# Kernel tuning notes

Measured on AMD Instinct MI355X. Metric: run time of the kernel, lower is better.

## Reference

```python
import jax, jax.numpy as jnp
import numpy as np

P = 1024   # total patches = B * n_patches
B = 32
NPATCH = 32
D = 64
EPS = 1e-6


def _mlp2(x, W1, b1, W2, b2):
    # Linear -> ReLU -> (Dropout p=0) -> Linear
    return jax.nn.relu(x @ W1 + b1) @ W2 + b2


def setup_inputs() -> dict:
    key = jax.random.key(0)
    ks = jax.random.split(key, 32)
    d = D
    inp = {}
    inp['x'] = jax.random.normal(ks[0], (65536, d), dtype=jnp.float32)
    inp['subgraphs_nodes_mapper'] = jax.random.randint(ks[1], (65536,), 0, 65536)
    inp['subgraphs_batch'] = jnp.sort(jax.random.randint(ks[2], (65536,), 0, P))
    inp['subgraphs_batch_row'] = jax.random.randint(ks[3], (16384,), 0, P)
    inp['subgraphs_batch_col'] = jax.random.randint(ks[4], (16384,), 0, P)
    inp['coarsen_edge_attr'] = jax.random.uniform(ks[5], (16384,), dtype=jnp.float32)
    s = 1.0 / np.sqrt(d)
    def W(k, shape):
        return jax.random.normal(k, shape, dtype=jnp.float32) * s
    # input_transform (Linear,ReLU,Linear,ReLU)
    inp['Wt1'] = W(ks[6], (d, d)); inp['bt1'] = jnp.zeros((d,), jnp.float32)
    inp['Wt2'] = W(ks[7], (d, d)); inp['bt2'] = jnp.zeros((d,), jnp.float32)
    # pre / post deepset (2 layers each)
    inp['Wpre1'] = W(ks[8], (d, d)); inp['bpre1'] = jnp.zeros((d,), jnp.float32)
    inp['Wpre2'] = W(ks[9], (d, d)); inp['bpre2'] = jnp.zeros((d,), jnp.float32)
    inp['Wpost1'] = W(ks[10], (d, d)); inp['bpost1'] = jnp.zeros((d,), jnp.float32)
    inp['Wpost2'] = W(ks[11], (d, d)); inp['bpost2'] = jnp.zeros((d,), jnp.float32)
    # linK / linV
    inp['Wk'] = W(ks[12], (d, d)); inp['bk'] = jnp.zeros((d,), jnp.float32)
    inp['Wv'] = W(ks[13], (d, d)); inp['bv'] = jnp.zeros((d,), jnp.float32)
    # attention-based readout seed
    inp['seed'] = jax.random.normal(ks[14], (d,), dtype=jnp.float32)
    # classifier: Linear(d, d//2), ReLU, Linear(d//2, num_classes)
    inp['Wc1'] = W(ks[15], (d, d // 2)); inp['bc1'] = jnp.zeros((d // 2,), jnp.float32)
    inp['Wc2'] = W(ks[16], (d // 2, 10)); inp['bc2'] = jnp.zeros((10,), jnp.float32)
    return inp


def reference(x, subgraphs_nodes_mapper, subgraphs_batch, subgraphs_batch_row,
              subgraphs_batch_col, coarsen_edge_attr,
              Wt1, bt1, Wt2, bt2,
              Wpre1, bpre1, Wpre2, bpre2,
              Wpost1, bpost1, Wpost2, bpost2,
              Wk, bk, Wv, bv, seed,
              Wc1, bc1, Wc2, bc2):
    seg = jax.ops.segment_sum
    row, col, batch = subgraphs_batch_row, subgraphs_batch_col, subgraphs_batch

    # input_transform then gather onto subgraph-combined node set
    h = jax.nn.relu(jax.nn.relu(x @ Wt1 + bt1) @ Wt2 + bt2)
    hs = h[subgraphs_nodes_mapper]                        # [N, d]

    # symmetric random-walk normalization of coarsened edge weights
    deg = seg(coarsen_edge_attr, row, num_segments=P)
    dinv = jnp.where(deg > 0, jax.lax.rsqrt(jnp.maximum(deg, EPS)), 0.0)
    attr = dinv[row] * coarsen_edge_attr * dinv[col]      # [E]

    # Q: pre-deepset -> scatter-sum per patch -> post-deepset
    Q = _mlp2(hs, Wpre1, bpre1, Wpre2, bpre2)
    Qs = seg(Q, batch, num_segments=P)                    # [P, d]
    Qs = _mlp2(Qs, Wpost1, bpost1, Wpost2, bpost2)

    # K: linear proj, scatter-mean per patch; V: linear proj (node level)
    K = hs @ Wk + bk
    cnt = seg(jnp.ones_like(K[:, 0]), batch, num_segments=P)
    Ks = seg(K, batch, num_segments=P) / jnp.maximum(cnt, 1.0)[:, None]
    V = hs @ Wv + bv

    # relu kernel feature maps
    Qk = jax.nn.relu(Qs)                                  # [P, d]
    Kk = jax.nn.relu(K)                                   # [N, d]
    Ksk = jax.nn.relu(Ks)                                 # [P, d]

    # linear attention state per patch: M_p = sum_{i in p} k_i v_i^T
    M = seg(Kk[:, :, None] * V[:, None, :], batch, num_segments=P)  # [P, d, d]
    # random-walk message / key propagation on coarsened patch graph
    M = M + seg(attr[:, None, None] * M[col], row, num_segments=P)
    Kagg = Ksk + seg(attr[:, None] * Ksk[col], row, num_segments=P)

    # kernelized attention readout per patch
    num = jnp.einsum('pd,pde->pe', Qk, M)
    den = jnp.sum(Qk * Kagg, axis=-1)
    out = num / (den[:, None] + EPS)                      # [P, d]

    # (B p) d -> B p d, attention-based set readout with learned seed
    out = out.reshape(B, NPATCH, D)
    scores = jax.nn.softmax((out @ seed) / jnp.sqrt(jnp.float32(D)), axis=1)
    pooled = jnp.einsum('bp,bpd->bd', scores, out)        # [B, d]

    # classifier
    logits = jax.nn.relu(pooled @ Wc1 + bc1) @ Wc2 + bc2  # [B, num_classes]
    return logits
```

## Files before the change

kernel.cpp:

```cpp
#include <hip/hip_runtime.h>
#include <cstddef>

#define NND  65536
#define PP   1024
#define EE   16384
#define CAP  88
#define TJ2  32
#define EPSF 1e-6f

typedef unsigned int   u32;
typedef unsigned short u16;
typedef __attribute__((ext_vector_type(8))) short bf16x8;
typedef __attribute__((ext_vector_type(4))) float f32x4;

__device__ __forceinline__ u16 f2bf(float f) {
    u32 u = __float_as_uint(f);
    u += 0x7fffu + ((u >> 16) & 1u);
    return (u16)(u >> 16);
}
__device__ __forceinline__ float bflo(u32 u) { return __uint_as_float(u << 16); }
__device__ __forceinline__ float bfhi(u32 u) { return __uint_as_float(u & 0xffff0000u); }
__device__ __forceinline__ float bf1(u16 v)  { return __uint_as_float(((u32)v) << 16); }
__device__ __forceinline__ u32 relu2(u32 v) {
    u32 mask = ((v & 0x80008000u) >> 15) * 0xFFFFu;
    return v & ~mask;
}


__global__ void patch_bounds_kernel(const int* __restrict__ batch, int* __restrict__ start) {
    int i = blockIdx.x * blockDim.x + threadIdx.x;
    if (i >= NND) return;
    int b  = batch[i];
    int bp = (i == 0) ? -1 : batch[i - 1];
    for (int p = bp + 1; p <= b; ++p) start[p] = i;
    if (i == NND - 1) {
        for (int p = b + 1; p <= PP; ++p) start[p] = NND;
    }
}

__global__ void edge_hist_kernel(const int* __restrict__ row, const int* __restrict__ col,
                                 const float* __restrict__ attr,
                                 float* __restrict__ deg, int* __restrict__ colcnt) {
    int e = blockIdx.x * blockDim.x + threadIdx.x;
    if (e >= EE) return;
    atomicAdd(&deg[row[e]], attr[e]);
    atomicAdd(&colcnt[col[e]], 1);
}

__global__ void scan_dinv_kernel(const int* __restrict__ colcnt, int* __restrict__ col_start,
                                 const float* __restrict__ deg, float* __restrict__ dinv) {
    __shared__ int s[PP];
    int t = threadIdx.x;
    s[t] = colcnt[t];
    float dg = deg[t];
    dinv[t] = (dg > 0.f) ? rsqrtf(fmaxf(dg, EPSF)) : 0.f;
    __syncthreads();
    for (int off = 1; off < PP; off <<= 1) {
        int v = (t >= off) ? s[t - off] : 0;
        __syncthreads();
        s[t] += v;
        __syncthreads();
    }
    col_start[t + 1] = s[t];
    if (t == 0) col_start[0] = 0;
}

__global__ void edge_scatter_kernel(const int* __restrict__ col, const int* __restrict__ col_start,
                                    int* __restrict__ colfill, int* __restrict__ edge_perm) {
    int e = blockIdx.x * blockDim.x + threadIdx.x;
    if (e >= EE) return;
    int c = col[e];
    int pos = col_start[c] + atomicAdd(&colfill[c], 1);
    edge_perm[pos] = e;
}

__global__ __launch_bounds__(256)
void pack_w_kernel(const float* W0, const float* W1, const float* W2, const float* W3,
                   const float* W4, const float* W5, const float* W6, const float* W7,
                   u16* __restrict__ out) {
    const float* Ws[8] = {W0, W1, W2, W3, W4, W5, W6, W7};
    const float* W = Ws[blockIdx.x];
    u16* dst = out + (size_t)blockIdx.x * 4096;
    int t = threadIdx.x;
    for (int idx = t; idx < 512; idx += 256) {
        int f = idx >> 6, l = idx & 63;
        int kk = f >> 2, nt = f & 3;
        int g = l >> 4, m = l & 15;
#pragma unroll
        for (int j = 0; j < 8; ++j) {
            int k = kk * 32 + g * 8 + j;
            int n = nt * 16 + m;
            dst[idx * 8 + j] = f2bf(W[k * 64 + n]);
        }
    }
}


__device__ __forceinline__ void stage_f32(const float* __restrict__ in, u16* s, int row0, int t) {
    int r = t >> 2, c = t & 3;
    const float4* src = (const float4*)(in + (size_t)(row0 + r) * 64 + c * 16);
    char* sb = (char*)s + r * 128;
    int swz = (r & 7) << 4;
#pragma unroll
    for (int q4 = 0; q4 < 4; ++q4) {
        float4 v = src[q4];
        u32 p0 = (u32)f2bf(v.x) | ((u32)f2bf(v.y) << 16);
        u32 p1 = (u32)f2bf(v.z) | ((u32)f2bf(v.w) << 16);
        int pc = c * 8 + q4 * 2;
        *(u32*)(sb + ((pc * 4) ^ swz))       = p0;
        *(u32*)(sb + (((pc + 1) * 4) ^ swz)) = p1;
    }
}

__device__ __forceinline__ void stage_bf16_gather(const u16* __restrict__ h,
                                                  const int* __restrict__ gmap,
                                                  u16* s, int row0, int t) {
    int r = t >> 2, c = t & 3;
    int sr = gmap[row0 + r];
    const uint4* src = (const uint4*)(h + (size_t)sr * 64) + c * 2;
    uint4 a = src[0], b = src[1];
    char* sb = (char*)s + r * 128;
    int swz = (r & 7) << 4;
    *(uint4*)(sb + ((c * 32) ^ swz))      = a;
    *(uint4*)(sb + ((c * 32 + 16) ^ swz)) = b;
}

template <bool RELU>
__device__ __forceinline__ void gemm_layer(const u16* src, u16* dst,
                                           const u16* __restrict__ Wp,
                                           const float* __restrict__ bias,
                                           int wv, int lane) {
    int g = lane >> 4, m = lane & 15;
    int arow = wv * 16 + m;
    const char* sb = (const char*)src + arow * 128;
    int aswz = (arow & 7) << 4;
    bf16x8 a0 = *(const bf16x8*)(sb + ((g * 16) ^ aswz));
    bf16x8 a1 = *(const bf16x8*)(sb + ((64 + g * 16) ^ aswz));
    const bf16x8* wp = (const bf16x8*)Wp;
#pragma unroll
    for (int ntile = 0; ntile < 4; ++ntile) {
        float bv = bias[ntile * 16 + m];
        f32x4 acc = {bv, bv, bv, bv};
        acc = __builtin_amdgcn_mfma_f32_16x16x32_bf16(a0, wp[(0 * 4 + ntile) * 64 + lane], acc, 0, 0, 0);
        acc = __builtin_amdgcn_mfma_f32_16x16x32_bf16(a1, wp[(1 * 4 + ntile) * 64 + lane], acc, 0, 0, 0);
        int col = ntile * 16 + m;
#pragma unroll
        for (int rg = 0; rg < 4; ++rg) {
            float v = acc[rg];
            if (RELU) v = fmaxf(v, 0.f);
            int rr = wv * 16 + g * 4 + rg;
            *(u16*)((char*)dst + rr * 128 + ((2 * col) ^ ((rr & 7) << 4))) = f2bf(v);
        }
    }
}

__device__ __forceinline__ void copy_out_bf16(const u16* s, u16* __restrict__ g, int row0, int t) {
    int r = t >> 2, c = t & 3;
    const char* sb = (const char*)s + r * 128;
    int swz = (r & 7) << 4;
    uint4 a = *(const uint4*)(sb + ((c * 32) ^ swz));
    uint4 b = *(const uint4*)(sb + ((c * 32 + 16) ^ swz));
    uint4* dst = (uint4*)(g + (size_t)(row0 + r) * 64) + c * 2;
    dst[0] = a; dst[1] = b;
}

__global__ __launch_bounds__(256)
void mfma_mlp2_kernel(const float* __restrict__ in,
                      const u16* __restrict__ Wp1, const float* __restrict__ b1,
                      const u16* __restrict__ Wp2, const float* __restrict__ b2,
                      u16* __restrict__ out) {
    __shared__ __align__(16) u16 xs[4096];
    __shared__ __align__(16) u16 ys[4096];
    int t = threadIdx.x, lane = t & 63, wv = t >> 6;
    int row0 = blockIdx.x * 64;
    stage_f32(in, xs, row0, t);
    gemm_layer<true>(xs, ys, Wp1, b1, wv, lane);
    gemm_layer<true>(ys, xs, Wp2, b2, wv, lane);
    copy_out_bf16(xs, out, row0, t);
}

__global__ __launch_bounds__(256)
void qkv_mfma_kernel(const u16* __restrict__ h, const int* __restrict__ gmap,
                     const u16* __restrict__ Wpk, const float* __restrict__ bk,
                     const u16* __restrict__ Wpv, const float* __restrict__ bv,
                     const u16* __restrict__ Wp1, const float* __restrict__ bp1,
                     const u16* __restrict__ Wp2, const float* __restrict__ bp2,
                     u16* __restrict__ Kout, u16* __restrict__ Vout, u16* __restrict__ Qout) {
    __shared__ __align__(16) u16 xs[4096];
    __shared__ __align__(16) u16 ys[4096];
    int t = threadIdx.x, lane = t & 63, wv = t >> 6;
    int row0 = blockIdx.x * 64;
    stage_bf16_gather(h, gmap, xs, row0, t);
    gemm_layer<false>(xs, ys, Wpk, bk, wv, lane);
    copy_out_bf16(ys, Kout, row0, t);
    gemm_layer<false>(xs, ys, Wpv, bv, wv, lane);
    copy_out_bf16(ys, Vout, row0, t);
    gemm_layer<true>(xs, ys, Wp1, bp1, wv, lane);
    gemm_layer<false>(ys, xs, Wp2, bp2, wv, lane);
    copy_out_bf16(xs, Qout, row0, t);
}

__global__ __launch_bounds__(256)
void patch_reduce_kernel(const u16* __restrict__ Qn, const u16* __restrict__ K,
                         const int* __restrict__ start,
                         float* __restrict__ Qs_raw, float* __restrict__ Ksk) {
    __shared__ float qred[8][64], kred[8][64];
    int p = blockIdx.x, t = threadIdx.x;
    int w = t & 31, s = t >> 5;
    int i0 = start[p], i1 = start[p + 1];
    float qa0 = 0.f, qa1 = 0.f, ka0 = 0.f, ka1 = 0.f;
    for (int i = i0 + s; i < i1; i += 8) {
        u32 qv = ((const u32*)(Qn + (size_t)i * 64))[w];
        u32 kv = ((const u32*)(K  + (size_t)i * 64))[w];
        qa0 += bflo(qv); qa1 += bfhi(qv);
        ka0 += bflo(kv); ka1 += bfhi(kv);
    }
    qred[s][w * 2] = qa0; qred[s][w * 2 + 1] = qa1;
    kred[s][w * 2] = ka0; kred[s][w * 2 + 1] = ka1;
    __syncthreads();
    if (t < 64) {
        float q = 0.f, k = 0.f;
#pragma unroll
        for (int z = 0; z < 8; ++z) { q += qred[z][t]; k += kred[z][t]; }
        Qs_raw[(size_t)p * 64 + t] = q;
        int cnt = i1 - i0;
        Ksk[(size_t)p * 64 + t] = fmaxf(k / (float)max(cnt, 1), 0.f);
    }
}

__global__ __launch_bounds__(256)
void attn2_kernel(const u16* __restrict__ Qkb, const u16* __restrict__ Kb,
                  const u16* __restrict__ Vb, const float* __restrict__ Kskb,
                  const int* __restrict__ e_row, const float* __restrict__ e_attr,
                  const int* __restrict__ edge_perm, const int* __restrict__ col_start,
                  const int* __restrict__ patch_start, const float* __restrict__ dinv,
                  float* __restrict__ num, float* __restrict__ Kagg) {
    __shared__ u16   Ks[CAP * 66];
    __shared__ u16   Vs[CAP * 66];
    __shared__ u16   Qs[TJ2 * 66];
    __shared__ float accS[TJ2 * 64];
    __shared__ float dots[4][CAP];
    __shared__ float coef[TJ2];
    __shared__ int   trow[TJ2];
    __shared__ float Ksc[64];
    int c = blockIdx.x, t = threadIdx.x, wv = t >> 6, lane = t & 63;
    int e0 = col_start[c], e1 = col_start[c + 1];
    int ntgt = e1 - e0 + 1;
    int i0 = patch_start[c], i1 = patch_start[c + 1];
    float dc = dinv[c];
    if (t < 64) Ksc[t] = Kskb[(size_t)c * 64 + t];

    for (int tc = 0; tc < ntgt; tc += TJ2) {
        int mj = min(TJ2, ntgt - tc);
        __syncthreads();
        if (t < mj) {
            int j = tc + t; int p; float cf;
            if (j == 0) { p = c; cf = 1.f; }
            else { int e = edge_perm[e0 + j - 1]; p = e_row[e]; cf = dinv[p] * e_attr[e] * dc; }
            trow[t] = p; coef[t] = cf;
        }
        for (int idx = t; idx < mj * 64; idx += 256) accS[idx] = 0.f;
        __syncthreads();
        for (int idx = t; idx < mj * 32; idx += 256) {
            int j = idx >> 5, q = idx & 31;
            u32 v = ((const u32*)(Qkb + (size_t)trow[j] * 64))[q];
            *(u32*)&Qs[j * 66 + q * 2] = v;
        }
        for (int ic = i0; ic < i1; ic += CAP) {
            int nc = min(CAP, i1 - ic);
            __syncthreads();
            for (int idx = t; idx < nc * 8; idx += 256) {
                int i = idx >> 3, q = idx & 7;
                uint4 kv = *((const uint4*)(Kb + (size_t)(ic + i) * 64) + q);
                uint4 vv = *((const uint4*)(Vb + (size_t)(ic + i) * 64) + q);
                u32* kd = (u32*)&Ks[i * 66 + q * 8];
                kd[0] = relu2(kv.x); kd[1] = relu2(kv.y);
                kd[2] = relu2(kv.z); kd[3] = relu2(kv.w);
                u32* vd = (u32*)&Vs[i * 66 + q * 8];
                vd[0] = vv.x; vd[1] = vv.y; vd[2] = vv.z; vd[3] = vv.w;
            }
            __syncthreads();
            for (int j = wv; j < mj; j += 4) {
                for (int ib = 0; ib < nc; ib += 64) {
                    int i = ib + lane;
                    if (i < nc) {
                        float dot = 0.f;
                        const u32* kr = (const u32*)&Ks[i * 66];
                        const u32* qr = (const u32*)&Qs[j * 66];
#pragma unroll 8
                        for (int q = 0; q < 32; ++q) {
                            u32 kw = kr[q], qw = qr[q];
                            dot = fmaf(bflo(qw), bflo(kw), dot);
                            dot = fmaf(bfhi(qw), bfhi(kw), dot);
                        }
                        dots[wv][i] = dot;
                    }
                }
                float out = 0.f;
#pragma unroll 4
                for (int i = 0; i < nc; ++i)
                    out = fmaf(dots[wv][i], bf1(Vs[i * 66 + lane]), out);
                accS[j * 64 + lane] += out;
            }
        }
        __syncthreads();
        for (int idx = t; idx < mj * 64; idx += 256) {
            int j = idx >> 6, d = idx & 63;
            float cf = coef[j];
            atomicAdd(&num[(size_t)trow[j] * 64 + d],  cf * accS[j * 64 + d]);
            atomicAdd(&Kagg[(size_t)trow[j] * 64 + d], cf * Ksc[d]);
        }
    }
}

__global__ __launch_bounds__(64)
void final_kernel(const float* __restrict__ num, const u16* __restrict__ Qk,
                  const float* __restrict__ Kagg, const float* __restrict__ seed,
                  const float* __restrict__ Wc1, const float* __restrict__ bc1,
                  const float* __restrict__ Wc2, const float* __restrict__ bc2,
                  float* __restrict__ logits) {
    __shared__ float s_out[32][65];
    __shared__ float s_rd[32], s_sc[32], s_pool[64], s_c1[32], s_seed[64];
    int b = blockIdx.x, t = threadIdx.x;
    s_seed[t] = seed[t];
    if (t < 32) {
        int p = b * 32 + t;
        float den = 0.f;
        for (int d = 0; d < 64; ++d)
            den = fmaf(bf1(Qk[(size_t)p * 64 + d]), Kagg[(size_t)p * 64 + d], den);
        s_rd[t] = 1.f / (den + EPSF);
    }
    __syncthreads();
    for (int p = 0; p < 32; ++p)
        s_out[p][t] = num[(size_t)(b * 32 + p) * 64 + t] * s_rd[p];
    __syncthreads();
    if (t < 32) {
        float sc = 0.f;
        for (int d = 0; d < 64; ++d) sc = fmaf(s_out[t][d], s_seed[d], sc);
        s_sc[t] = sc * 0.125f;
    }
    __syncthreads();
    if (t == 0) {
        float mx = -1e30f;
        for (int p = 0; p < 32; ++p) mx = fmaxf(mx, s_sc[p]);
        float sm = 0.f;
        for (int p = 0; p < 32; ++p) { float e = expf(s_sc[p] - mx); s_sc[p] = e; sm += e; }
        float inv = 1.f / sm;
        for (int p = 0; p < 32; ++p) s_sc[p] *= inv;
    }
    __syncthreads();
    {
        float pa = 0.f;
        for (int p = 0; p < 32; ++p) pa = fmaf(s_sc[p], s_out[p][t], pa);
        s_pool[t] = pa;
    }
    __syncthreads();
    if (t < 32) {
        float a = bc1[t];
        for (int d = 0; d < 64; ++d) a = fmaf(s_pool[d], Wc1[d * 32 + t], a);
        s_c1[t] = fmaxf(a, 0.f);
    }
    __syncthreads();
    if (t < 10) {
        float a = bc2[t];
        for (int j = 0; j < 32; ++j) a = fmaf(s_c1[j], Wc2[j * 10 + t], a);
        logits[b * 10 + t] = a;
    }
}


extern "C" void kernel_launch(void* const* d_in, const int* in_sizes, int n_in,
                              void* d_out, int out_size, void* d_ws, size_t ws_size,
                              hipStream_t stream) {
    const float* x      = (const float*)d_in[0];
    const int*   mapper = (const int*)d_in[1];
    const int*   batch  = (const int*)d_in[2];
    const int*   e_row  = (const int*)d_in[3];
    const int*   e_col  = (const int*)d_in[4];
    const float* e_attr = (const float*)d_in[5];
    const float* Wt1 = (const float*)d_in[6],  *bt1 = (const float*)d_in[7];
    const float* Wt2 = (const float*)d_in[8],  *bt2 = (const float*)d_in[9];
    const float* Wpre1 = (const float*)d_in[10], *bpre1 = (const float*)d_in[11];
    const float* Wpre2 = (const float*)d_in[12], *bpre2 = (const float*)d_in[13];
    const float* Wpost1 = (const float*)d_in[14], *bpost1 = (const float*)d_in[15];
    const float* Wpost2 = (const float*)d_in[16], *bpost2 = (const float*)d_in[17];
    const float* Wk = (const float*)d_in[18], *bk = (const float*)d_in[19];
    const float* Wv = (const float*)d_in[20], *bv = (const float*)d_in[21];
    const float* seed = (const float*)d_in[22];
    const float* Wc1 = (const float*)d_in[23], *bc1 = (const float*)d_in[24];
    const float* Wc2 = (const float*)d_in[25], *bc2 = (const float*)d_in[26];
    float* logits = (float*)d_out;

    char* w = (char*)d_ws;
    const size_t NB2 = (size_t)NND * 64 * 2;
    u16* hb  = (u16*)w;             w += NB2;
    u16* Kb  = (u16*)w;             w += NB2;
    u16* Vb  = (u16*)w;             w += NB2;
    u16* Qnb = (u16*)w;             w += NB2;
    u16* Wp  = (u16*)w;             w += 8 * 4096 * 2;
    u16* Qkb = (u16*)w;             w += PP * 64 * 2;
    float* numb   = (float*)w;      w += PP * 64 * 4;
    float* Kagg   = (float*)w;      w += PP * 64 * 4;
    float* Qs_raw = (float*)w;      w += PP * 64 * 4;
    float* Kskb   = (float*)w;      w += PP * 64 * 4;
    float* deg    = (float*)w;      w += PP * 4;
    int*   colcnt = (int*)w;        w += PP * 4;
    int*   colfill= (int*)w;        w += PP * 4;
    float* dinv   = (float*)w;      w += PP * 4;
    int* patch_start = (int*)w;     w += (PP + 1) * 4;
    int* col_start   = (int*)w;     w += (PP + 1) * 4;
    int* edge_perm   = (int*)w;     w += EE * 4;

    hipMemsetAsync(numb, 0, 2 * PP * 64 * sizeof(float), stream);
    hipMemsetAsync(deg, 0, 3 * PP * sizeof(int), stream);

    patch_bounds_kernel<<<NND / 256, 256, 0, stream>>>(batch, patch_start);
    edge_hist_kernel<<<EE / 256, 256, 0, stream>>>(e_row, e_col, e_attr, deg, colcnt);
    scan_dinv_kernel<<<1, PP, 0, stream>>>(colcnt, col_start, deg, dinv);
    edge_scatter_kernel<<<EE / 256, 256, 0, stream>>>(e_col, col_start, colfill, edge_perm);

    pack_w_kernel<<<8, 256, 0, stream>>>(Wt1, Wt2, Wk, Wv, Wpre1, Wpre2, Wpost1, Wpost2, Wp);

    mfma_mlp2_kernel<<<NND / 64, 256, 0, stream>>>(
        x, Wp + 0 * 4096, bt1, Wp + 1 * 4096, bt2, hb);
    qkv_mfma_kernel<<<NND / 64, 256, 0, stream>>>(
        hb, mapper, Wp + 2 * 4096, bk, Wp + 3 * 4096, bv,
        Wp + 4 * 4096, bpre1, Wp + 5 * 4096, bpre2, Kb, Vb, Qnb);
    patch_reduce_kernel<<<PP, 256, 0, stream>>>(Qnb, Kb, patch_start, Qs_raw, Kskb);
    mfma_mlp2_kernel<<<PP / 64, 256, 0, stream>>>(
        Qs_raw, Wp + 6 * 4096, bpost1, Wp + 7 * 4096, bpost2, Qkb);
    attn2_kernel<<<PP, 256, 0, stream>>>(Qkb, Kb, Vb, Kskb, e_row, e_attr, edge_perm,
                                         col_start, patch_start, dinv, numb, Kagg);
    final_kernel<<<32, 64, 0, stream>>>(numb, Qkb, Kagg, seed, Wc1, bc1, Wc2, bc2, logits);
}
```

Before: 199.3 us.

## Fuse setup kernels and fold patch reductions into QKV GEMM epilogue

```diff
diff --git a/kernel.cpp b/kernel.cpp
--- a/kernel.cpp
+++ b/kernel.cpp
@@ -27,71 +27,73 @@
 }
 
 
-__global__ void patch_bounds_kernel(const int* __restrict__ batch, int* __restrict__ start) {
-    int i = blockIdx.x * blockDim.x + threadIdx.x;
-    if (i >= NND) return;
-    int b  = batch[i];
-    int bp = (i == 0) ? -1 : batch[i - 1];
-    for (int p = bp + 1; p <= b; ++p) start[p] = i;
-    if (i == NND - 1) {
-        for (int p = b + 1; p <= PP; ++p) start[p] = NND;
-    }
-}
-
-__global__ void edge_hist_kernel(const int* __restrict__ row, const int* __restrict__ col,
-                                 const float* __restrict__ attr,
-                                 float* __restrict__ deg, int* __restrict__ colcnt) {
-    int e = blockIdx.x * blockDim.x + threadIdx.x;
-    if (e >= EE) return;
-    atomicAdd(&deg[row[e]], attr[e]);
-    atomicAdd(&colcnt[col[e]], 1);
-}
-
-__global__ void scan_dinv_kernel(const int* __restrict__ colcnt, int* __restrict__ col_start,
-                                 const float* __restrict__ deg, float* __restrict__ dinv) {
-    __shared__ int s[PP];
+__global__ __launch_bounds__(256)
+void setup_a_kernel(const int* __restrict__ batch, int* __restrict__ start,
+                    const float* W0, const float* W1, const float* W2, const float* W3,
+                    const float* W4, const float* W5, const float* W6, const float* W7,
+                    u16* __restrict__ wout) {
+    int blk = blockIdx.x, t = threadIdx.x;
+    if (blk < 256) {
+        int i = blk * 256 + t;
+        int b  = batch[i];
+        int bp = (i == 0) ? -1 : batch[i - 1];
+        for (int p = bp + 1; p <= b; ++p) start[p] = i;
+        if (i == NND - 1) {
+            for (int p = b + 1; p <= PP; ++p) start[p] = NND;
+        }
+    } else {
+        const float* Ws[8] = {W0, W1, W2, W3, W4, W5, W6, W7};
+        const float* W = Ws[blk - 256];
+        u16* dst = wout + (size_t)(blk - 256) * 4096;
+        for (int idx = t; idx < 512; idx += 256) {
+            int f = idx >> 6, l = idx & 63;
+            int kk = f >> 2, nt = f & 3;
+            int g = l >> 4, m = l & 15;
+#pragma unroll
+            for (int j = 0; j < 8; ++j) {
+                int k = kk * 32 + g * 8 + j;
+                int n = nt * 16 + m;
+                dst[idx * 8 + j] = f2bf(W[k * 64 + n]);
+            }
+        }
+    }
+}
+
+
+__global__ __launch_bounds__(1024)
+void setup_edges_kernel(const int* __restrict__ e_row, const int* __restrict__ e_col,
+                        const float* __restrict__ e_attr,
+                        int* __restrict__ col_start, int* __restrict__ edge_perm,
+                        float* __restrict__ dinv_g) {
+    __shared__ float sdeg[PP];
+    __shared__ int scc[PP], sfc[PP], stmp[PP];
     int t = threadIdx.x;
-    s[t] = colcnt[t];
-    float dg = deg[t];
-    dinv[t] = (dg > 0.f) ? rsqrtf(fmaxf(dg, EPSF)) : 0.f;
+    sdeg[t] = 0.f; scc[t] = 0; sfc[t] = 0;
+    __syncthreads();
+    for (int e = t; e < EE; e += 1024) {
+        atomicAdd(&sdeg[e_row[e]], e_attr[e]);
+        atomicAdd(&scc[e_col[e]], 1);
+    }
+    __syncthreads();
+    float dg = sdeg[t];
+    dinv_g[t] = (dg > 0.f) ? rsqrtf(fmaxf(dg, EPSF)) : 0.f;
+    stmp[t] = scc[t];
     __syncthreads();
     for (int off = 1; off < PP; off <<= 1) {
-        int v = (t >= off) ? s[t - off] : 0;
+        int v = (t >= off) ? stmp[t - off] : 0;
         __syncthreads();
-        s[t] += v;
+        stmp[t] += v;
         __syncthreads();
     }
-    col_start[t + 1] = s[t];
+    col_start[t + 1] = stmp[t];
     if (t == 0) col_start[0] = 0;
-}
-
-__global__ void edge_scatter_kernel(const int* __restrict__ col, const int* __restrict__ col_start,
-                                    int* __restrict__ colfill, int* __restrict__ edge_perm) {
-    int e = blockIdx.x * blockDim.x + threadIdx.x;
-    if (e >= EE) return;
-    int c = col[e];
-    int pos = col_start[c] + atomicAdd(&colfill[c], 1);
-    edge_perm[pos] = e;
-}
-
-__global__ __launch_bounds__(256)
-void pack_w_kernel(const float* W0, const float* W1, const float* W2, const float* W3,
-                   const float* W4, const float* W5, const float* W6, const float* W7,
-                   u16* __restrict__ out) {
-    const float* Ws[8] = {W0, W1, W2, W3, W4, W5, W6, W7};
-    const float* W = Ws[blockIdx.x];
-    u16* dst = out + (size_t)blockIdx.x * 4096;
-    int t = threadIdx.x;
-    for (int idx = t; idx < 512; idx += 256) {
-        int f = idx >> 6, l = idx & 63;
-        int kk = f >> 2, nt = f & 3;
-        int g = l >> 4, m = l & 15;
-#pragma unroll
-        for (int j = 0; j < 8; ++j) {
-            int k = kk * 32 + g * 8 + j;
-            int n = nt * 16 + m;
-            dst[idx * 8 + j] = f2bf(W[k * 64 + n]);
-        }
+    int excl = stmp[t] - scc[t];
+    scc[t] = excl;
+    __syncthreads();
+    for (int e = t; e < EE; e += 1024) {
+        int c = e_col[e];
+        int pos = scc[c] + atomicAdd(&sfc[c], 1);
+        edge_perm[pos] = e;
     }
 }
 
@@ -164,11 +166,34 @@
     dst[0] = a; dst[1] = b;
 }
 
+__device__ __forceinline__ void seg_reduce_tile(const u16* tile, const int* __restrict__ batch,
+                                                int row0, int wv, int lane,
+                                                float* __restrict__ gout) {
+    float s = 0.f;
+    int cur = batch[row0 + wv * 16];
+#pragma unroll
+    for (int r = 0; r < 16; ++r) {
+        int row = wv * 16 + r;
+        const char* rb = (const char*)tile + row * 128;
+        float v = bf1(*(const u16*)(rb + ((2 * lane) ^ ((row & 7) << 4))));
+        int b = batch[row0 + row];
+        if (b != cur) {
+            atomicAdd(&gout[(size_t)cur * 64 + lane], s);
+            s = 0.f; cur = b;
+        }
+        s += v;
+    }
+    atomicAdd(&gout[(size_t)cur * 64 + lane], s);
+}
+
+template <bool KSK>
 __global__ __launch_bounds__(256)
 void mfma_mlp2_kernel(const float* __restrict__ in,
                       const u16* __restrict__ Wp1, const float* __restrict__ b1,
                       const u16* __restrict__ Wp2, const float* __restrict__ b2,
-                      u16* __restrict__ out) {
+                      u16* __restrict__ out,
+                      const int* __restrict__ pstart, const float* __restrict__ Ksum,
+                      u16* __restrict__ Kskb) {
     __shared__ __align__(16) u16 xs[4096];
     __shared__ __align__(16) u16 ys[4096];
     int t = threadIdx.x, lane = t & 63, wv = t >> 6;
@@ -177,15 +202,26 @@
     gemm_layer<true>(xs, ys, Wp1, b1, wv, lane);
     gemm_layer<true>(ys, xs, Wp2, b2, wv, lane);
     copy_out_bf16(xs, out, row0, t);
+    if (KSK) {
+        for (int idx = t; idx < 4096; idx += 256) {
+            int r = idx >> 6, d = idx & 63;
+            int p = row0 + r;
+            int cnt = pstart[p + 1] - pstart[p];
+            float kv = Ksum[(size_t)p * 64 + d] / (float)max(cnt, 1);
+            Kskb[(size_t)p * 64 + d] = f2bf(fmaxf(kv, 0.f));
+        }
+    }
 }
 
 __global__ __launch_bounds__(256)
 void qkv_mfma_kernel(const u16* __restrict__ h, const int* __restrict__ gmap,
+                     const int* __restrict__ batch,
                      const u16* __restrict__ Wpk, const float* __restrict__ bk,
                      const u16* __restrict__ Wpv, const float* __restrict__ bv,
                      const u16* __restrict__ Wp1, const float* __restrict__ bp1,
                      const u16* __restrict__ Wp2, const float* __restrict__ bp2,
-                     u16* __restrict__ Kout, u16* __restrict__ Vout, u16* __restrict__ Qout) {
+                     u16* __restrict__ Kout, u16* __restrict__ Vout,
+                     float* __restrict__ Qsum, float* __restrict__ Ksum) {
     __shared__ __align__(16) u16 xs[4096];
     __shared__ __align__(16) u16 ys[4096];
     int t = threadIdx.x, lane = t & 63, wv = t >> 6;
@@ -193,44 +229,17 @@
     stage_bf16_gather(h, gmap, xs, row0, t);
     gemm_layer<false>(xs, ys, Wpk, bk, wv, lane);
     copy_out_bf16(ys, Kout, row0, t);
+    seg_reduce_tile(ys, batch, row0, wv, lane, Ksum);
     gemm_layer<false>(xs, ys, Wpv, bv, wv, lane);
     copy_out_bf16(ys, Vout, row0, t);
     gemm_layer<true>(xs, ys, Wp1, bp1, wv, lane);
     gemm_layer<false>(ys, xs, Wp2, bp2, wv, lane);
-    copy_out_bf16(xs, Qout, row0, t);
-}
-
-__global__ __launch_bounds__(256)
-void patch_reduce_kernel(const u16* __restrict__ Qn, const u16* __restrict__ K,
-                         const int* __restrict__ start,
-                         float* __restrict__ Qs_raw, float* __restrict__ Ksk) {
-    __shared__ float qred[8][64], kred[8][64];
-    int p = blockIdx.x, t = threadIdx.x;
-    int w = t & 31, s = t >> 5;
-    int i0 = start[p], i1 = start[p + 1];
-    float qa0 = 0.f, qa1 = 0.f, ka0 = 0.f, ka1 = 0.f;
-    for (int i = i0 + s; i < i1; i += 8) {
-        u32 qv = ((const u32*)(Qn + (size_t)i * 64))[w];
-        u32 kv = ((const u32*)(K  + (size_t)i * 64))[w];
-        qa0 += bflo(qv); qa1 += bfhi(qv);
-        ka0 += bflo(kv); ka1 += bfhi(kv);
-    }
-    qred[s][w * 2] = qa0; qred[s][w * 2 + 1] = qa1;
-    kred[s][w * 2] = ka0; kred[s][w * 2 + 1] = ka1;
-    __syncthreads();
-    if (t < 64) {
-        float q = 0.f, k = 0.f;
-#pragma unroll
-        for (int z = 0; z < 8; ++z) { q += qred[z][t]; k += kred[z][t]; }
-        Qs_raw[(size_t)p * 64 + t] = q;
-        int cnt = i1 - i0;
-        Ksk[(size_t)p * 64 + t] = fmaxf(k / (float)max(cnt, 1), 0.f);
-    }
+    seg_reduce_tile(xs, batch, row0, wv, lane, Qsum);
 }
 
 __global__ __launch_bounds__(256)
 void attn2_kernel(const u16* __restrict__ Qkb, const u16* __restrict__ Kb,
-                  const u16* __restrict__ Vb, const float* __restrict__ Kskb,
+                  const u16* __restrict__ Vb, const u16* __restrict__ Kskb,
                   const int* __restrict__ e_row, const float* __restrict__ e_attr,
                   const int* __restrict__ edge_perm, const int* __restrict__ col_start,
                   const int* __restrict__ patch_start, const float* __restrict__ dinv,
@@ -248,7 +257,7 @@
     int ntgt = e1 - e0 + 1;
     int i0 = patch_start[c], i1 = patch_start[c + 1];
     float dc = dinv[c];
-    if (t < 64) Ksc[t] = Kskb[(size_t)c * 64 + t];
+    if (t < 64) Ksc[t] = bf1(Kskb[(size_t)c * 64 + t]);
 
     for (int tc = 0; tc < ntgt; tc += TJ2) {
         int mj = min(TJ2, ntgt - tc);
@@ -396,39 +405,33 @@
     u16* hb  = (u16*)w;             w += NB2;
     u16* Kb  = (u16*)w;             w += NB2;
     u16* Vb  = (u16*)w;             w += NB2;
-    u16* Qnb = (u16*)w;             w += NB2;
     u16* Wp  = (u16*)w;             w += 8 * 4096 * 2;
     u16* Qkb = (u16*)w;             w += PP * 64 * 2;
-    float* numb   = (float*)w;      w += PP * 64 * 4;
-    float* Kagg   = (float*)w;      w += PP * 64 * 4;
-    float* Qs_raw = (float*)w;      w += PP * 64 * 4;
-    float* Kskb   = (float*)w;      w += PP * 64 * 4;
-    float* deg    = (float*)w;      w += PP * 4;
-    int*   colcnt = (int*)w;        w += PP * 4;
-    int*   colfill= (int*)w;        w += PP * 4;
-    float* dinv   = (float*)w;      w += PP * 4;
+    u16* Kskb= (u16*)w;             w += PP * 64 * 2;
+    float* Qsum  = (float*)w;       w += PP * 64 * 4;
+    float* Ksum  = (float*)w;       w += PP * 64 * 4;
+    float* numb  = (float*)w;       w += PP * 64 * 4;
+    float* Kagg  = (float*)w;       w += PP * 64 * 4;
+    float* dinv  = (float*)w;       w += PP * 4;
     int* patch_start = (int*)w;     w += (PP + 1) * 4;
     int* col_start   = (int*)w;     w += (PP + 1) * 4;
     int* edge_perm   = (int*)w;     w += EE * 4;
 
-    hipMemsetAsync(numb, 0, 2 * PP * 64 * sizeof(float), stream);
-    hipMemsetAsync(deg, 0, 3 * PP * sizeof(int), stream);
-
-    patch_bounds_kernel<<<NND / 256, 256, 0, stream>>>(batch, patch_start);
-    edge_hist_kernel<<<EE / 256, 256, 0, stream>>>(e_row, e_col, e_attr, deg, colcnt);
-    scan_dinv_kernel<<<1, PP, 0, stream>>>(colcnt, col_start, deg, dinv);
-    edge_scatter_kernel<<<EE / 256, 256, 0, stream>>>(e_col, col_start, colfill, edge_perm);
-
-    pack_w_kernel<<<8, 256, 0, stream>>>(Wt1, Wt2, Wk, Wv, Wpre1, Wpre2, Wpost1, Wpost2, Wp);
-
-    mfma_mlp2_kernel<<<NND / 64, 256, 0, stream>>>(
-        x, Wp + 0 * 4096, bt1, Wp + 1 * 4096, bt2, hb);
+    hipMemsetAsync(Qsum, 0, 4 * PP * 64 * sizeof(float), stream);
+
+    setup_a_kernel<<<264, 256, 0, stream>>>(batch, patch_start,
+        Wt1, Wt2, Wk, Wv, Wpre1, Wpre2, Wpost1, Wpost2, Wp);
+    setup_edges_kernel<<<1, 1024, 0, stream>>>(e_row, e_col, e_attr,
+                                               col_start, edge_perm, dinv);
+
+    mfma_mlp2_kernel<false><<<NND / 64, 256, 0, stream>>>(
+        x, Wp + 0 * 4096, bt1, Wp + 1 * 4096, bt2, hb, nullptr, nullptr, nullptr);
     qkv_mfma_kernel<<<NND / 64, 256, 0, stream>>>(
-        hb, mapper, Wp + 2 * 4096, bk, Wp + 3 * 4096, bv,
-        Wp + 4 * 4096, bpre1, Wp + 5 * 4096, bpre2, Kb, Vb, Qnb);
-    patch_reduce_kernel<<<PP, 256, 0, stream>>>(Qnb, Kb, patch_start, Qs_raw, Kskb);
-    mfma_mlp2_kernel<<<PP / 64, 256, 0, stream>>>(
-        Qs_raw, Wp + 6 * 4096, bpost1, Wp + 7 * 4096, bpost2, Qkb);
+        hb, mapper, batch, Wp + 2 * 4096, bk, Wp + 3 * 4096, bv,
+        Wp + 4 * 4096, bpre1, Wp + 5 * 4096, bpre2, Kb, Vb, Qsum, Ksum);
+    mfma_mlp2_kernel<true><<<PP / 64, 256, 0, stream>>>(
+        Qsum, Wp + 6 * 4096, bpost1, Wp + 7 * 4096, bpost2, Qkb,
+        patch_start, Ksum, Kskb);
     attn2_kernel<<<PP, 256, 0, stream>>>(Qkb, Kb, Vb, Kskb, e_row, e_attr, edge_perm,
                                          col_start, patch_start, dinv, numb, Kagg);
     final_kernel<<<32, 64, 0, stream>>>(numb, Qkb, Kagg, seed, Wc1, bc1, Wc2, bc2, logits);
```

Result: slower. 225.7 us (+13.2%).
